# Optimization experiments

Measured on AMD Instinct MI355X. Metric: run time of the kernel, lower is better.

The kernel has to match this reference:

```python
import jax, jax.numpy as jnp
import numpy as np

B = 256
# (Cin, Cout, K, Hout) for each of the 6 deformable conv layers; input is 33x33
_LAYERS = [(1, 16, 3, 31), (16, 32, 3, 29), (32, 16, 5, 25), (16, 16, 7, 19), (16, 8, 5, 15), (8, 4, 3, 13)]


def setup_inputs() -> dict:
    key = jax.random.key(0)
    ks = jax.random.split(key, 24)
    inp = {"x": jax.random.normal(ks[0], (B, 1, 33, 33), dtype=jnp.float32)}
    for i, (ci, co, k, ho) in enumerate(_LAYERS):
        inp[f"off{i+1}"] = jax.random.normal(ks[1 + i], (1, 2 * k * k, ho, ho), dtype=jnp.float32)
        inp[f"w{i+1}"] = jax.random.normal(ks[7 + i], (co, ci, k, k), dtype=jnp.float32) / float(np.sqrt(ci * k * k))
        inp[f"b{i+1}"] = jnp.zeros((co,), jnp.float32)
    inp["w7"] = jax.random.normal(ks[13], (13 * 13 * 4, 256), dtype=jnp.float32) / 26.0
    inp["b7"] = jnp.zeros((256,), jnp.float32)
    inp["w8"] = jax.random.normal(ks[14], (256, 10), dtype=jnp.float32) / 16.0
    inp["b8"] = jnp.zeros((10,), jnp.float32)
    inp["perm"] = jnp.arange(13 * 13, dtype=jnp.int32)  # fixed spatial permutation (perm_6.ordenar)
    return inp


def _deform_conv(x, offset, weight, bias):
    # torchvision DeformConv2d, stride=1, padding=0, fixed offsets shared across batch.
    Bn, Cin, H, W = x.shape
    Cout, _, K, _ = weight.shape
    Ho, Wo = offset.shape[-2], offset.shape[-1]
    K2 = K * K
    off = offset[0].reshape(K2, 2, Ho, Wo)  # channel layout: [2k]=dy, [2k+1]=dx
    ky, kx = jnp.meshgrid(jnp.arange(K), jnp.arange(K), indexing='ij')
    py = jnp.arange(Ho, dtype=x.dtype)[None, :, None] + ky.reshape(-1, 1, 1) + off[:, 0]  # [K2,Ho,Wo]
    px = jnp.arange(Wo, dtype=x.dtype)[None, None, :] + kx.reshape(-1, 1, 1) + off[:, 1]
    y0f = jnp.floor(py); x0f = jnp.floor(px)
    wy = py - y0f; wx = px - x0f
    y0 = y0f.astype(jnp.int32); x0 = x0f.astype(jnp.int32)
    xf = x.reshape(Bn, Cin, H * W)

    def gather(yi, xi):
        valid = ((yi >= 0) & (yi < H) & (xi >= 0) & (xi < W)).astype(x.dtype)
        idx = (jnp.clip(yi, 0, H - 1) * W + jnp.clip(xi, 0, W - 1)).reshape(-1)
        v = xf[:, :, idx].reshape(Bn, Cin, K2, Ho, Wo)
        return v * valid[None, None]

    s = (gather(y0, x0) * ((1 - wy) * (1 - wx))[None, None]
         + gather(y0, x0 + 1) * ((1 - wy) * wx)[None, None]
         + gather(y0 + 1, x0) * (wy * (1 - wx))[None, None]
         + gather(y0 + 1, x0 + 1) * (wy * wx)[None, None])  # [B,Cin,K2,Ho,Wo]
    out = jnp.einsum('bckhw,ock->bohw', s, weight.reshape(Cout, Cin, K2))
    return out + bias[None, :, None, None]


def reference(x, off1, off2, off3, off4, off5, off6,
              w1, b1, w2, b2, w3, b3, w4, b4, w5, b5, w6, b6,
              w7, b7, w8, b8, perm):
    offs = (off1, off2, off3, off4, off5, off6)
    ws = (w1, w2, w3, w4, w5, w6)
    bs = (b1, b2, b3, b4, b5, b6)
    for off, w, b in zip(offs, ws, bs):
        x = jax.nn.relu(_deform_conv(x, off, w, b))
    Bn = x.shape[0]
    x = x.reshape(Bn, 4, 13 * 13)[:, :, perm].reshape(Bn, -1)  # perm_6.ordenar as spatial permutation
    h = jax.nn.relu(x @ w7 + b7)
    return h @ w8 + b8
```

## Files before the change

kernel.cpp:

```cpp
#include <hip/hip_runtime.h>

template<int N> struct IC { static constexpr int val = N; };

struct WtArgs { const float* src[6]; int co[6], ci[6], k2[6], dstoff[6]; };

__global__ __launch_bounds__(256)
void transpose_weights(WtArgs a, float* __restrict__ dst0)
{
    const int L = blockIdx.x;
    const float* __restrict__ s = a.src[L];
    float* __restrict__ d = dst0 + a.dstoff[L];
    const int co = a.co[L], ci = a.ci[L], k2 = a.k2[L];
    const int n = co * ci * k2;
    for (int i = threadIdx.x; i < n; i += 256) {
        int k = i % k2;
        int c = (i / k2) % ci;
        int o = i / (k2 * ci);
        d[(k * ci + c) * co + o] = s[i];
    }
}

struct MetaArgs { const float* off[6]; int P[6], K[6], WO[6], H[6], W[6], base[6]; };

__global__ __launch_bounds__(256)
void build_meta(MetaArgs a, float* __restrict__ meta0)
{
    const int L = blockIdx.y;
    const float* __restrict__ off = a.off[L];
    const int P = a.P[L], K = a.K[L], WOv = a.WO[L], H = a.H[L], Wv = a.W[L];
    const int N = P * K * K;
    float* __restrict__ m = meta0 + (size_t)a.base[L] * 8;
    for (int e = blockIdx.x * 256 + threadIdx.x; e < N; e += gridDim.x * 256) {
        const int k = e / P, p = e - k * P;
        const int ho = p / WOv, wo = p - ho * WOv;
        const int ky = k / K, kx = k - ky * K;
        const float dy = off[(2 * k)     * P + p];
        const float dx = off[(2 * k + 1) * P + p];
        const float py = (float)(ho + ky) + dy;
        const float px = (float)(wo + kx) + dx;
        const float y0f = floorf(py), x0f = floorf(px);
        const float wy = py - y0f, wx = px - x0f;
        const int y0 = (int)y0f, x0 = (int)x0f;
        const int y1 = y0 + 1,  x1 = x0 + 1;
        const bool vy0 = ((unsigned)y0 < (unsigned)H);
        const bool vy1 = ((unsigned)y1 < (unsigned)H);
        const bool vx0 = ((unsigned)x0 < (unsigned)Wv);
        const bool vx1 = ((unsigned)x1 < (unsigned)Wv);
        const int cy0 = min(max(y0, 0), H - 1) * Wv;
        const int cy1 = min(max(y1, 0), H - 1) * Wv;
        const int cx0 = min(max(x0, 0), Wv - 1);
        const int cx1 = min(max(x1, 0), Wv - 1);
        int4 mi;
        mi.x = cy0 + cx0; mi.y = cy0 + cx1; mi.z = cy1 + cx0; mi.w = cy1 + cx1;
        float4 mw;
        mw.x = (vy0 && vx0) ? (1.f - wy) * (1.f - wx) : 0.f;
        mw.y = (vy0 && vx1) ? (1.f - wy) * wx         : 0.f;
        mw.z = (vy1 && vx0) ? wy * (1.f - wx)         : 0.f;
        mw.w = (vy1 && vx1) ? wy * wx                 : 0.f;
        *(int4*)(m + (size_t)e * 8)       = mi;
        *(float4*)(m + (size_t)e * 8 + 4) = mw;
    }
}

template<int CIN, int CINW, int COUT, int K, int H, int W, int HO, int WO,
         int S, int KSEG, int NT, int NCOMB, bool SPLITOUT, bool MET,
         int NSL = 1, int CINL = 0, int NCHS = 1, int KSPL = 1>
__global__ __launch_bounds__(NT)
void deform_lds(const float* __restrict__ x0, const float* __restrict__ x1,
                const float* __restrict__ x2, const float* __restrict__ x3,
                const float* __restrict__ off, const float* __restrict__ meta,
                const float* __restrict__ wT, const float* __restrict__ bias,
                float* __restrict__ y, size_t pstride)
{
    constexpr int K2 = K * K, HW = H * W, P = HO * WO;
    constexpr int PW = ((P + 63) / 64) * 64;
    constexpr int K2B  = (K2 + KSPL - 1) / KSPL;
    constexpr int KLEN = (K2B + KSEG - 1) / KSEG;
    constexpr int PSTR = (COUT % 2 == 0) ? COUT + 1 : COUT;
    static_assert(NT >= KSEG * PW, "NT too small for KSEG*PW");

    __shared__ __align__(16) float simg[HW * S];
    __shared__ float part[(KSEG > 1) ? (KSEG - 1) * P * PSTR : 1];

    const int tid = threadIdx.x;
    const int b   = blockIdx.x;
    const int hy  = SPLITOUT ? blockIdx.y : 0;
    const int hch = (KSPL > 1) ? (hy % NCHS) : hy;
    const int hk  = (KSPL > 1) ? (hy / NCHS) : 0;

    const size_t xoff = (size_t)b * CINW * HW + (SPLITOUT ? (size_t)hch * CIN * HW : 0);
    const float* xb  = x0 + xoff;
    const float* xb1 = (NCOMB >= 2) ? (x1 + xoff) : nullptr;
    const float* xb2 = (NCOMB >= 3) ? (x2 + xoff) : nullptr;
    const float* xb3 = (NCOMB >= 4) ? (x3 + xoff) : nullptr;
    for (int i = tid; i < CIN * HW; i += NT) {
        int c = i / HW, hw = i - c * HW;
        bool ok = true;
        if constexpr (SPLITOUT) ok = (hch * CIN + c < CINW);
        float v = 0.f;
        if (ok) {
            v = xb[i];
            if constexpr (NCOMB >= 2) v += xb1[i];
            if constexpr (NCOMB >= 3) v += xb2[i];
            if constexpr (NCOMB >= 4) v += xb3[i];
            if constexpr (NCOMB >= 2) v = fmaxf(v, 0.f);
        }
        simg[hw * S + c] = v;
    }
    __syncthreads();

    const int g  = tid / PW;
    const int p  = tid - g * PW;
    const int pc = (p < P) ? p : (P - 1);
    const bool active = (p < P);

    float acc[COUT];
#pragma unroll
    for (int o = 0; o < COUT; ++o) acc[o] = 0.f;

    if (g < KSEG) {
        if ((!SPLITOUT || hy == 0) && g == 0) {
#pragma unroll
            for (int o = 0; o < COUT; ++o) acc[o] = bias[o];
        }
        const int ho = pc / WO, wo = pc - ho * WO;
        const int kb   = hk * K2B + g * KLEN;
        const int kend = (KSPL > 1) ? min(K2, hk * K2B + K2B) : K2;

        auto run = [&](auto nc4tag) {
            constexpr int NC4 = decltype(nc4tag)::val;

            auto fma_block = [&](int i00, int i01, int i10, int i11,
                                 float w00, float w01, float w10, float w11,
                                 int kku) {
                const float* __restrict__ r00 = simg + i00 * S;
                const float* __restrict__ r01 = simg + i01 * S;
                const float* __restrict__ r10 = simg + i10 * S;
                const float* __restrict__ r11 = simg + i11 * S;
                const float* __restrict__ wk = wT + kku * (CINW * COUT)
                                             + (SPLITOUT ? hch * (CIN * COUT) : 0);
                if constexpr (CIN % 4 == 0) {
#pragma unroll
                    for (int c4 = 0; c4 < NC4; ++c4) {
                        const float4 v00 = *(const float4*)(r00 + c4 * 4);
                        const float4 v01 = *(const float4*)(r01 + c4 * 4);
                        const float4 v10 = *(const float4*)(r10 + c4 * 4);
                        const float4 v11 = *(const float4*)(r11 + c4 * 4);
                        float4 sa;
                        sa.x = fmaf(w00, v00.x, fmaf(w01, v01.x, fmaf(w10, v10.x, w11 * v11.x)));
                        sa.y = fmaf(w00, v00.y, fmaf(w01, v01.y, fmaf(w10, v10.y, w11 * v11.y)));
                        sa.z = fmaf(w00, v00.z, fmaf(w01, v01.z, fmaf(w10, v10.z, w11 * v11.z)));
                        sa.w = fmaf(w00, v00.w, fmaf(w01, v01.w, fmaf(w10, v10.w, w11 * v11.w)));
                        const float* __restrict__ wc = wk + (c4 * 4) * COUT;
#pragma unroll
                        for (int o = 0; o < COUT; ++o) acc[o] = fmaf(wc[o], sa.x, acc[o]);
#pragma unroll
                        for (int o = 0; o < COUT; ++o) acc[o] = fmaf(wc[COUT + o], sa.y, acc[o]);
#pragma unroll
                        for (int o = 0; o < COUT; ++o) acc[o] = fmaf(wc[2 * COUT + o], sa.z, acc[o]);
#pragma unroll
                        for (int o = 0; o < COUT; ++o) acc[o] = fmaf(wc[3 * COUT + o], sa.w, acc[o]);
                    }
                } else {
#pragma unroll
                    for (int c = 0; c < CIN; ++c) {
                        float sa = fmaf(w00, r00[c], fmaf(w01, r01[c],
                                   fmaf(w10, r10[c], w11 * r11[c])));
#pragma unroll
                        for (int o = 0; o < COUT; ++o)
                            acc[o] = fmaf(wk[c * COUT + o], sa, acc[o]);
                    }
                }
            };

            if constexpr (MET) {
                const int kf = (kb < K2) ? kb : (K2 - 1);
                int4   nmi = *(const int4*)  (meta + (size_t)(kf * P + pc) * 8);
                float4 nmw = *(const float4*)(meta + (size_t)(kf * P + pc) * 8 + 4);

#pragma unroll 1
                for (int j = 0; j < KLEN; ++j) {
                    const int k  = kb + j;
                    const int kk = (k < K2) ? k : (K2 - 1);
                    const int4   mi  = nmi;
                    const float4 mwv = nmw;
                    const int kn = (k + 1 < K2) ? (k + 1) : (K2 - 1);
                    nmi = *(const int4*)  (meta + (size_t)(kn * P + pc) * 8);
                    nmw = *(const float4*)(meta + (size_t)(kn * P + pc) * 8 + 4);

                    float w00 = mwv.x, w01 = mwv.y, w10 = mwv.z, w11 = mwv.w;
                    if constexpr (K2 % (KSEG * KSPL) != 0) {
                        const float kv = (k < kend) ? 1.f : 0.f;
                        w00 *= kv; w01 *= kv; w10 *= kv; w11 *= kv;
                    }
                    const int kku = __builtin_amdgcn_readfirstlane(kk);
                    fma_block(mi.x, mi.y, mi.z, mi.w, w00, w01, w10, w11, kku);
                }
            } else {
                const int kf = (kb < K2) ? kb : (K2 - 1);
                float ndy = off[(2 * kf)     * P + pc];
                float ndx = off[(2 * kf + 1) * P + pc];

#pragma unroll 1
                for (int j = 0; j < KLEN; ++j) {
                    const int k  = kb + j;
                    const int kk = (k < K2) ? k : (K2 - 1);
                    const float dy = ndy, dx = ndx;
                    const int kn = (k + 1 < K2) ? (k + 1) : (K2 - 1);
                    ndy = off[(2 * kn)     * P + pc];
                    ndx = off[(2 * kn + 1) * P + pc];

                    const int ky = kk / K, kx = kk - ky * K;
                    const float py = (float)(ho + ky) + dy;
                    const float px = (float)(wo + kx) + dx;
                    const float y0f = floorf(py), x0f = floorf(px);
                    const float wy = py - y0f, wx = px - x0f;
                    const int y0 = (int)y0f, x0 = (int)x0f;
                    const int y1 = y0 + 1,  x1i = x0 + 1;
                    const bool vy0 = ((unsigned)y0  < (unsigned)H);
                    const bool vy1 = ((unsigned)y1  < (unsigned)H);
                    const bool vx0 = ((unsigned)x0  < (unsigned)W);
                    const bool vx1 = ((unsigned)x1i < (unsigned)W);
                    const int cy0 = min(max(y0, 0), H - 1) * W;
                    const int cy1 = min(max(y1, 0), H - 1) * W;
                    const int cx0 = min(max(x0, 0), W - 1);
                    const int cx1 = min(max(x1i, 0), W - 1);
                    float w00 = (vy0 && vx0) ? (1.f - wy) * (1.f - wx) : 0.f;
                    float w01 = (vy0 && vx1) ? (1.f - wy) * wx         : 0.f;
                    float w10 = (vy1 && vx0) ? wy * (1.f - wx)         : 0.f;
                    float w11 = (vy1 && vx1) ? wy * wx                 : 0.f;
                    if constexpr (K2 % (KSEG * KSPL) != 0) {
                        const float kv = (k < kend) ? 1.f : 0.f;
                        w00 *= kv; w01 *= kv; w10 *= kv; w11 *= kv;
                    }
                    const int kku = __builtin_amdgcn_readfirstlane(kk);
                    fma_block(cy0 + cx0, cy0 + cx1, cy1 + cx0, cy1 + cx1,
                              w00, w01, w10, w11, kku);
                }
            }
        };

        if constexpr (SPLITOUT && CINL > 0) {
            if (hch == NSL - 1) run(IC<(CINL + 3) / 4>{});
            else                run(IC<(CIN + 3) / 4>{});
        } else {
            run(IC<(CIN + 3) / 4>{});
        }

        if (g > 0 && active) {
#pragma unroll
            for (int o = 0; o < COUT; ++o)
                part[(g - 1) * (P * PSTR) + p * PSTR + o] = acc[o];
        }
    }

    if constexpr (KSEG > 1) __syncthreads();

    if (g == 0 && active) {
        if constexpr (KSEG > 1) {
#pragma unroll
            for (int gg = 1; gg < KSEG; ++gg)
#pragma unroll
                for (int o = 0; o < COUT; ++o)
                    acc[o] += part[(gg - 1) * (P * PSTR) + p * PSTR + o];
        }
        float* yb = y + (SPLITOUT ? (size_t)hy * pstride : 0) + (size_t)b * COUT * P;
#pragma unroll
        for (int o = 0; o < COUT; ++o)
            yb[o * P + p] = SPLITOUT ? acc[o] : fmaxf(acc[o], 0.f);
    }
}

__global__ __launch_bounds__(256)
void fc_head(const float* __restrict__ x6, const float* __restrict__ w7,
             const float* __restrict__ b7, const float* __restrict__ w8,
             const float* __restrict__ b8, const int* __restrict__ perm,
             float* __restrict__ out)
{
    constexpr int F = 676;
    __shared__ float sx[F];
    __shared__ float sh[256];

    const int tid = threadIdx.x;
    const int b   = blockIdx.x;

    for (int i = tid; i < F; i += 256) {
        int c = i / 169, p = i - c * 169;
        sx[i] = x6[(size_t)b * F + c * 169 + perm[p]];
    }
    __syncthreads();

    float a0 = 0.f, a1 = 0.f, a2 = 0.f, a3 = 0.f;
#pragma unroll 2
    for (int i = 0; i < 169; ++i) {
        a0 = fmaf(sx[i],       w7[(size_t)i * 256 + tid],         a0);
        a1 = fmaf(sx[169 + i], w7[(size_t)(169 + i) * 256 + tid], a1);
        a2 = fmaf(sx[338 + i], w7[(size_t)(338 + i) * 256 + tid], a2);
        a3 = fmaf(sx[507 + i], w7[(size_t)(507 + i) * 256 + tid], a3);
    }
    sh[tid] = fmaxf(b7[tid] + ((a0 + a1) + (a2 + a3)), 0.f);
    __syncthreads();

    if (tid < 10) {
        float a = b8[tid];
#pragma unroll 8
        for (int j = 0; j < 256; ++j)
            a = fmaf(sh[j], w8[j * 10 + tid], a);
        out[(size_t)b * 10 + tid] = a;
    }
}

extern "C" void kernel_launch(void* const* d_in, const int* in_sizes, int n_in,
                              void* d_out, int out_size, void* d_ws, size_t ws_size,
                              hipStream_t stream)
{
    const float* x    = (const float*)d_in[0];
    const float* off1 = (const float*)d_in[1];
    const float* w1   = (const float*)d_in[2];
    const float* b1   = (const float*)d_in[3];
    const float* off2 = (const float*)d_in[4];
    const float* w2   = (const float*)d_in[5];
    const float* b2   = (const float*)d_in[6];
    const float* off3 = (const float*)d_in[7];
    const float* w3   = (const float*)d_in[8];
    const float* b3   = (const float*)d_in[9];
    const float* off4 = (const float*)d_in[10];
    const float* w4   = (const float*)d_in[11];
    const float* b4   = (const float*)d_in[12];
    const float* off5 = (const float*)d_in[13];
    const float* w5   = (const float*)d_in[14];
    const float* b5   = (const float*)d_in[15];
    const float* off6 = (const float*)d_in[16];
    const float* w6   = (const float*)d_in[17];
    const float* b6   = (const float*)d_in[18];
    const float* w7   = (const float*)d_in[19];
    const float* b7   = (const float*)d_in[20];
    const float* w8   = (const float*)d_in[21];
    const float* b8   = (const float*)d_in[22];
    const int*   perm = (const int*)d_in[23];
    float* out = (float*)d_out;

    const int woff[6] = {0, 144, 4752, 17552, 30096, 33296};
    float* ws   = (float*)d_ws;
    float* wt   = ws;
    float* buf0 = ws + 33792;
    float* buf1 = buf0 + 3936256;

    float* a1   = buf0;
    float* a2   = buf1;
    float* p1L2 = ws + 13419520;
    float* a3   = buf0;
    float* p1L3 = ws + 10859520;
    float* a4p0 = buf1;
    float* a5   = buf0;
    float* a6   = buf1;
    float* meta = ws + 20308992;

    const int mbase[6] = {0, 8649, 16218, 31843, 49532, 55157};
    const int MTOT = 56678;

    const bool splitL3 = (ws_size >= (size_t)13419520 * sizeof(float));
    const bool splitL2 = (ws_size >= (size_t)20308992 * sizeof(float));
    const bool metaOK  = (ws_size >= (size_t)(20308992 + MTOT * 8) * sizeof(float));
    const bool split3  = (ws_size >= (size_t)24245248 * sizeof(float));
    const size_t X      = 10825728;
    const size_t pstrL2 = (size_t)(p1L2 - a2);
    const size_t pstrL4 = 1478656;

    WtArgs wa;
    wa.src[0] = w1; wa.src[1] = w2; wa.src[2] = w3;
    wa.src[3] = w4; wa.src[4] = w5; wa.src[5] = w6;
    const int cos[6] = {16, 32, 16, 16, 8, 4};
    const int cis[6] = {1, 16, 32, 16, 16, 8};
    const int k2s[6] = {9, 9, 25, 49, 25, 9};
    for (int i = 0; i < 6; ++i) {
        wa.co[i] = cos[i]; wa.ci[i] = cis[i];
        wa.k2[i] = k2s[i]; wa.dstoff[i] = woff[i];
    }
    transpose_weights<<<dim3(6), dim3(256), 0, stream>>>(wa, wt);

    const dim3 g1(256), g2(256, 2), g3(256, 3), g4(256, 4);

    if (metaOK) {
        MetaArgs ma;
        ma.off[0] = off1; ma.off[1] = off2; ma.off[2] = off3;
        ma.off[3] = off4; ma.off[4] = off5; ma.off[5] = off6;
        const int Ps[6]  = {961, 841, 625, 361, 225, 169};
        const int Ks[6]  = {3, 3, 5, 7, 5, 3};
        const int WOs[6] = {31, 29, 25, 19, 15, 13};
        const int Hs[6]  = {33, 31, 29, 25, 19, 15};
        const int Ws_[6] = {33, 31, 29, 25, 19, 15};
        for (int i = 0; i < 6; ++i) {
            ma.P[i] = Ps[i]; ma.K[i] = Ks[i]; ma.WO[i] = WOs[i];
            ma.H[i] = Hs[i]; ma.W[i] = Ws_[i]; ma.base[i] = mbase[i];
        }
        build_meta<<<dim3(64, 6), dim3(256), 0, stream>>>(ma, meta);

        deform_lds< 1,  1, 16, 3, 33, 33, 31, 31,  1, 1, 1024, 1, false, true>
            <<<g1, dim3(1024), 0, stream>>>(x, nullptr, nullptr, nullptr, off1, meta + (size_t)mbase[0]*8, wt + woff[0], b1, a1, 0);
        deform_lds< 8, 16, 32, 3, 31, 31, 29, 29, 12, 1,  896, 1, true,  true>
            <<<g2, dim3(896),  0, stream>>>(a1, nullptr, nullptr, nullptr, off2, meta + (size_t)mbase[1]*8, wt + woff[1], b2, a2, pstrL2);

        if (split3) {
            deform_lds<12, 32, 16, 5, 29, 29, 25, 25, 12, 1,  640, 2, true,  true, 3, 8>
                <<<g3, dim3(640),  0, stream>>>(a2, p1L2, nullptr, nullptr, off3, meta + (size_t)mbase[2]*8, wt + woff[2], b3, a3, X);
            deform_lds< 8, 16, 16, 7, 25, 25, 19, 19, 12, 1,  384, 3, true,  true, 1, 0, 2, 2>
                <<<g4, dim3(384),  0, stream>>>(a3, a3 + X, a3 + 2 * X, nullptr, off4, meta + (size_t)mbase[3]*8, wt + woff[3], b4, a4p0, pstrL4);
            deform_lds<16, 16,  8, 5, 19, 19, 15, 15, 20, 4, 1024, 4, false, true>
                <<<g1, dim3(1024), 0, stream>>>(a4p0, a4p0 + pstrL4, a4p0 + 2 * pstrL4, a4p0 + 3 * pstrL4, off5, meta + (size_t)mbase[4]*8, wt + woff[4], b5, a5, 0);
        } else {
            deform_lds<16, 32, 16, 5, 29, 29, 25, 25, 20, 1,  640, 2, true,  true>
                <<<g2, dim3(640),  0, stream>>>(a2, p1L2, nullptr, nullptr, off3, meta + (size_t)mbase[2]*8, wt + woff[2], b3, a3, X);
            deform_lds< 8, 16, 16, 7, 25, 25, 19, 19, 12, 2,  768, 2, true,  true>
                <<<g2, dim3(768),  0, stream>>>(a3, a3 + X, nullptr, nullptr, off4, meta + (size_t)mbase[3]*8, wt + woff[3], b4, a4p0, pstrL4);
            deform_lds<16, 16,  8, 5, 19, 19, 15, 15, 20, 4, 1024, 2, false, true>
                <<<g1, dim3(1024), 0, stream>>>(a4p0, a4p0 + pstrL4, nullptr, nullptr, off5, meta + (size_t)mbase[4]*8, wt + woff[4], b5, a5, 0);
        }

        deform_lds< 8,  8,  4, 3, 15, 15, 13, 13, 12, 5,  960, 1, false, true>
            <<<g1, dim3(960),  0, stream>>>(a5, nullptr, nullptr, nullptr, off6, meta + (size_t)mbase[5]*8, wt + woff[5], b6, a6, 0);
    } else {
        deform_lds< 1,  1, 16, 3, 33, 33, 31, 31,  1, 1, 1024, 1, false, false>
            <<<g1, dim3(1024), 0, stream>>>(x, nullptr, nullptr, nullptr, off1, nullptr, wt + woff[0], b1, a1, 0);
        if (splitL2) {
            deform_lds< 8, 16, 32, 3, 31, 31, 29, 29, 12, 1, 1024, 1, true, false>
                <<<g2, dim3(1024), 0, stream>>>(a1, nullptr, nullptr, nullptr, off2, nullptr, wt + woff[1], b2, a2, pstrL2);
        } else {
            deform_lds<16, 16, 32, 3, 31, 31, 29, 29, 20, 1, 1024, 1, false, false>
                <<<g1, dim3(1024), 0, stream>>>(a1, nullptr, nullptr, nullptr, off2, nullptr, wt + woff[1], b2, a2, 0);
        }
        if (splitL3) {
            if (splitL2) {
                deform_lds<16, 32, 16, 5, 29, 29, 25, 25, 20, 1, 1024, 2, true, false>
                    <<<g2, dim3(1024), 0, stream>>>(a2, p1L2, nullptr, nullptr, off3, nullptr, wt + woff[2], b3, a3, X);
            } else {
                deform_lds<16, 32, 16, 5, 29, 29, 25, 25, 20, 1, 1024, 1, true, false>
                    <<<g2, dim3(1024), 0, stream>>>(a2, nullptr, nullptr, nullptr, off3, nullptr, wt + woff[2], b3, a3, X);
            }
            deform_lds< 8, 16, 16, 7, 25, 25, 19, 19, 12, 2,  768, 2, true, false>
                <<<g2, dim3(768),  0, stream>>>(a3, a3 + X, nullptr, nullptr, off4, nullptr, wt + woff[3], b4, a4p0, pstrL4);
        } else {
            deform_lds<32, 32, 16, 5, 29, 29, 25, 25, 36, 1, 1024, 1, false, false>
                <<<g1, dim3(1024), 0, stream>>>(a2, nullptr, nullptr, nullptr, off3, nullptr, wt + woff[2], b3, a3, 0);
            deform_lds< 8, 16, 16, 7, 25, 25, 19, 19, 12, 2,  768, 1, true, false>
                <<<g2, dim3(768),  0, stream>>>(a3, nullptr, nullptr, nullptr, off4, nullptr, wt + woff[3], b4, a4p0, pstrL4);
        }
        deform_lds<16, 16,  8, 5, 19, 19, 15, 15, 20, 4, 1024, 2, false, false>
            <<<g1, dim3(1024), 0, stream>>>(a4p0, a4p0 + pstrL4, nullptr, nullptr, off5, nullptr, wt + woff[4], b5, a5, 0);
        deform_lds< 8,  8,  4, 3, 15, 15, 13, 13, 12, 5,  960, 1, false, false>
            <<<g1, dim3(960),  0, stream>>>(a5, nullptr, nullptr, nullptr, off6, nullptr, wt + woff[5], b6, a6, 0);
    }

    fc_head<<<dim3(256), dim3(256), 0, stream>>>(a6, w7, b7, w8, b8, perm, out);
}
```

Before: 280.2 us.

## Split FC head reduction across 1024 threads and revert layer-4 split to two halves

The fc_head kernel now launches 1024 threads per block. Each group of 256 threads reduces one quarter of the 676 input features, and the partial sums are combined through shared memory. This raises parallelism and memory-level concurrency for the w7 GEMV. Separately, in the split3 path, layer 4 returns to a two-way output split with 768 threads that reads three input partials, and layer 5 goes back to consuming two partials. That drops the four-way split configuration, trading layer-4 grid size for a cheaper layer 5.

New measurement: 237.5 us. 1.18x faster.

```diff
diff --git a/kernel.cpp b/kernel.cpp
--- a/kernel.cpp
+++ b/kernel.cpp
@@ -271,7 +271,7 @@
     }
 }
 
-__global__ __launch_bounds__(256)
+__global__ __launch_bounds__(1024)
 void fc_head(const float* __restrict__ x6, const float* __restrict__ w7,
              const float* __restrict__ b7, const float* __restrict__ w8,
              const float* __restrict__ b8, const int* __restrict__ perm,
@@ -279,34 +279,39 @@
 {
     constexpr int F = 676;
     __shared__ float sx[F];
+    __shared__ float ps[3][256];
     __shared__ float sh[256];
 
     const int tid = threadIdx.x;
     const int b   = blockIdx.x;
-
-    for (int i = tid; i < F; i += 256) {
+    const int j   = tid & 255;
+    const int fq  = tid >> 8;
+
+    for (int i = tid; i < F; i += 1024) {
         int c = i / 169, p = i - c * 169;
         sx[i] = x6[(size_t)b * F + c * 169 + perm[p]];
     }
     __syncthreads();
 
-    float a0 = 0.f, a1 = 0.f, a2 = 0.f, a3 = 0.f;
-#pragma unroll 2
-    for (int i = 0; i < 169; ++i) {
-        a0 = fmaf(sx[i],       w7[(size_t)i * 256 + tid],         a0);
-        a1 = fmaf(sx[169 + i], w7[(size_t)(169 + i) * 256 + tid], a1);
-        a2 = fmaf(sx[338 + i], w7[(size_t)(338 + i) * 256 + tid], a2);
-        a3 = fmaf(sx[507 + i], w7[(size_t)(507 + i) * 256 + tid], a3);
-    }
-    sh[tid] = fmaxf(b7[tid] + ((a0 + a1) + (a2 + a3)), 0.f);
+    const int f0 = fq * 169;
+    float a = 0.f;
+#pragma unroll 4
+    for (int i = 0; i < 169; ++i)
+        a = fmaf(sx[f0 + i], w7[(size_t)(f0 + i) * 256 + j], a);
+
+    if (fq > 0) ps[fq - 1][j] = a;
     __syncthreads();
 
+    if (fq == 0)
+        sh[j] = fmaxf(b7[j] + ((a + ps[0][j]) + (ps[1][j] + ps[2][j])), 0.f);
+    __syncthreads();
+
     if (tid < 10) {
-        float a = b8[tid];
+        float acc8 = b8[tid];
 #pragma unroll 8
-        for (int j = 0; j < 256; ++j)
-            a = fmaf(sh[j], w8[j * 10 + tid], a);
-        out[(size_t)b * 10 + tid] = a;
+        for (int jj = 0; jj < 256; ++jj)
+            acc8 = fmaf(sh[jj], w8[jj * 10 + tid], acc8);
+        out[(size_t)b * 10 + tid] = acc8;
     }
 }
 
@@ -379,7 +384,7 @@
     }
     transpose_weights<<<dim3(6), dim3(256), 0, stream>>>(wa, wt);
 
-    const dim3 g1(256), g2(256, 2), g3(256, 3), g4(256, 4);
+    const dim3 g1(256), g2(256, 2), g3(256, 3);
 
     if (metaOK) {
         MetaArgs ma;
@@ -404,19 +409,17 @@
         if (split3) {
             deform_lds<12, 32, 16, 5, 29, 29, 25, 25, 12, 1,  640, 2, true,  true, 3, 8>
                 <<<g3, dim3(640),  0, stream>>>(a2, p1L2, nullptr, nullptr, off3, meta + (size_t)mbase[2]*8, wt + woff[2], b3, a3, X);
-            deform_lds< 8, 16, 16, 7, 25, 25, 19, 19, 12, 1,  384, 3, true,  true, 1, 0, 2, 2>
-                <<<g4, dim3(384),  0, stream>>>(a3, a3 + X, a3 + 2 * X, nullptr, off4, meta + (size_t)mbase[3]*8, wt + woff[3], b4, a4p0, pstrL4);
-            deform_lds<16, 16,  8, 5, 19, 19, 15, 15, 20, 4, 1024, 4, false, true>
-                <<<g1, dim3(1024), 0, stream>>>(a4p0, a4p0 + pstrL4, a4p0 + 2 * pstrL4, a4p0 + 3 * pstrL4, off5, meta + (size_t)mbase[4]*8, wt + woff[4], b5, a5, 0);
+            deform_lds< 8, 16, 16, 7, 25, 25, 19, 19, 12, 2,  768, 3, true,  true>
+                <<<g2, dim3(768),  0, stream>>>(a3, a3 + X, a3 + 2 * X, nullptr, off4, meta + (size_t)mbase[3]*8, wt + woff[3], b4, a4p0, pstrL4);
         } else {
             deform_lds<16, 32, 16, 5, 29, 29, 25, 25, 20, 1,  640, 2, true,  true>
                 <<<g2, dim3(640),  0, stream>>>(a2, p1L2, nullptr, nullptr, off3, meta + (size_t)mbase[2]*8, wt + woff[2], b3, a3, X);
             deform_lds< 8, 16, 16, 7, 25, 25, 19, 19, 12, 2,  768, 2, true,  true>
                 <<<g2, dim3(768),  0, stream>>>(a3, a3 + X, nullptr, nullptr, off4, meta + (size_t)mbase[3]*8, wt + woff[3], b4, a4p0, pstrL4);
-            deform_lds<16, 16,  8, 5, 19, 19, 15, 15, 20, 4, 1024, 2, false, true>
-                <<<g1, dim3(1024), 0, stream>>>(a4p0, a4p0 + pstrL4, nullptr, nullptr, off5, meta + (size_t)mbase[4]*8, wt + woff[4], b5, a5, 0);
-        }
-
+        }
+
+        deform_lds<16, 16,  8, 5, 19, 19, 15, 15, 20, 4, 1024, 2, false, true>
+            <<<g1, dim3(1024), 0, stream>>>(a4p0, a4p0 + pstrL4, nullptr, nullptr, off5, meta + (size_t)mbase[4]*8, wt + woff[4], b5, a5, 0);
         deform_lds< 8,  8,  4, 3, 15, 15, 13, 13, 12, 5,  960, 1, false, true>
             <<<g1, dim3(960),  0, stream>>>(a5, nullptr, nullptr, nullptr, off6, meta + (size_t)mbase[5]*8, wt + woff[5], b6, a6, 0);
     } else {
@@ -451,5 +454,5 @@
             <<<g1, dim3(960),  0, stream>>>(a5, nullptr, nullptr, nullptr, off6, nullptr, wt + woff[5], b6, a6, 0);
     }
 
-    fc_head<<<dim3(256), dim3(256), 0, stream>>>(a6, w7, b7, w8, b8, perm, out);
+    fc_head<<<dim3(256), dim3(1024), 0, stream>>>(a6, w7, b7, w8, b8, perm, out);
 }
```
